# Performance work log

Measured on AMD Instinct MI355X. Metric: run time of the kernel, lower is better.

The kernel has to match this reference:

```python
import jax, jax.numpy as jnp
import numpy as np

K = 3
PAD = 1
K2 = K * K


def _deform_conv(x, offset, w, b):
    """torchvision-style DeformConv2d, stride=1, padding=1, kernel=3, dilation=1.
    x: [B,C,H,W]; offset: [B,2*K2,H,W] (per-tap (dy,dx) interleaved); w: [O,C,K,K]; b: [O].
    """
    B, C, H, W = x.shape
    # kernel tap offsets relative to center (padding=1 => taps at -1,0,1)
    ky = (jnp.arange(K) - PAD).astype(x.dtype)
    kx = (jnp.arange(K) - PAD).astype(x.dtype)
    ky = jnp.repeat(ky, K)   # [K2]
    kx = jnp.tile(kx, K)     # [K2]

    off = offset.reshape(B, K2, 2, H, W)
    # sampling coordinates: [B,K2,H,W]
    yy = off[:, :, 0] + ky[None, :, None, None] + jnp.arange(H, dtype=x.dtype)[None, None, :, None]
    xx = off[:, :, 1] + kx[None, :, None, None] + jnp.arange(W, dtype=x.dtype)[None, None, None, :]

    def sample_one(img, yb, xb):  # img [C,H,W]; yb,xb [K2,H,W]
        y0 = jnp.floor(yb)
        x0 = jnp.floor(xb)
        dy = yb - y0
        dx = xb - x0
        y0i = y0.astype(jnp.int32)
        x0i = x0.astype(jnp.int32)
        img_flat = img.reshape(C, -1)

        def gather(yi, xi):
            valid = (yi >= 0) & (yi < H) & (xi >= 0) & (xi < W)
            idx = jnp.clip(yi, 0, H - 1) * W + jnp.clip(xi, 0, W - 1)
            v = jnp.take(img_flat, idx.reshape(-1), axis=1).reshape(C, K2, H, W)
            return v * valid[None].astype(img.dtype)

        v00 = gather(y0i, x0i)
        v01 = gather(y0i, x0i + 1)
        v10 = gather(y0i + 1, x0i)
        v11 = gather(y0i + 1, x0i + 1)
        w00 = ((1 - dy) * (1 - dx))[None]
        w01 = ((1 - dy) * dx)[None]
        w10 = (dy * (1 - dx))[None]
        w11 = (dy * dx)[None]
        return v00 * w00 + v01 * w01 + v10 * w10 + v11 * w11  # [C,K2,H,W]

    samp = jax.vmap(sample_one)(x, yy, xx)  # [B,C,K2,H,W]
    wr = w.reshape(w.shape[0], C, K2)       # [O,C,K2]
    out = jnp.einsum('bckhw,ock->bohw', samp, wr)
    return out + b[None, :, None, None]


def setup_inputs() -> dict:
    key = jax.random.key(0)
    ks = jax.random.split(key, 8)
    B, Cin, H, W = 16, 256, 32, 32
    Ch, NC = 256, 1000
    fan1 = Cin * K2
    fan2 = Ch * K2
    return {
        'x': jax.random.normal(ks[0], (B, Cin, H, W), jnp.float32),
        'offset': jax.random.normal(ks[1], (B, 2 * K2, H, W), jnp.float32),
        'w1': jax.random.normal(ks[2], (Ch, Cin, K, K), jnp.float32) / np.sqrt(fan1),
        'b1': jnp.zeros((Ch,), jnp.float32),
        'w2': jax.random.normal(ks[3], (Ch, Ch, K, K), jnp.float32) / np.sqrt(fan2),
        'b2': jnp.zeros((Ch,), jnp.float32),
        'fc_w': jax.random.normal(ks[4], (NC, Ch), jnp.float32) / np.sqrt(Ch),
        'fc_b': jnp.zeros((NC,), jnp.float32),
    }


def reference(x, offset, w1, b1, w2, b2, fc_w, fc_b):
    h = jax.nn.relu(_deform_conv(x, offset, w1, b1))
    h = jax.nn.relu(_deform_conv(h, offset, w2, b2))
    pooled = h.mean(axis=(2, 3))            # adaptive_avg_pool2d to (1,1) then flatten
    return pooled @ fc_w.T + fc_b
```

## Files before the change

### kernel.cpp

```cpp
#include <hip/hip_runtime.h>

#define B_     16
#define C_     256
#define H_     32
#define W_     32
#define O_     256
#define K2_    9
#define HW_    1024
#define KTOT   2304
#define NPOS   16384
#define NCHUNK 288
#define NT     256

typedef __bf16 bf16;
typedef __attribute__((ext_vector_type(8))) __bf16 bf16x8;
typedef __attribute__((ext_vector_type(4))) float  f32x4;

__device__ __forceinline__ void gload_lds16(const bf16* g, bf16* l) {
    __builtin_amdgcn_global_load_lds(
        (const __attribute__((address_space(1))) void*)g,
        (__attribute__((address_space(3))) void*)l, 16, 0, 0);
}

__device__ __forceinline__ float4 load4(const float* p, int t) {
    return ((const float4*)p)[t];
}
__device__ __forceinline__ float4 load4(const bf16* p, int t) {
    const ushort4 u = ((const ushort4*)p)[t];
    float4 f;
    f.x = __uint_as_float((unsigned)u.x << 16);
    f.y = __uint_as_float((unsigned)u.y << 16);
    f.z = __uint_as_float((unsigned)u.z << 16);
    f.w = __uint_as_float((unsigned)u.w << 16);
    return f;
}

__global__ __launch_bounds__(256) void prep_w(
    const float* __restrict__ w, bf16* __restrict__ Wt)
{
    const int o    = blockIdx.x;
    const int om   = o >> 7, o128 = o & 127;
    for (int k = threadIdx.x; k < KTOT; k += 256) {
        const int cg  = k / 72;
        const int rem = k - cg * 72;
        const int tap = rem >> 3;
        const int cl  = rem & 7;
        const int c   = cg * 8 + cl;
        const int chunk = cg * 9 + tap;
        Wt[(((size_t)om * NCHUNK + chunk) * 128 + o128) * 8 + cl] =
            (bf16)w[((size_t)o * C_ + c) * K2_ + tap];
    }
}

template<typename T>
__global__ __launch_bounds__(256) void sample_kernel(
    const T* __restrict__ src, size_t c_stride, size_t b_stride,
    const float* __restrict__ off,
    bf16* __restrict__ S)
{
    __shared__ float4 xs4[2][1152];

    const int tid = threadIdx.x;
    const int cg  = blockIdx.x & 31;
    const int rq  = (blockIdx.x >> 5) & 3;
    const int b   = blockIdx.x >> 7;

    #pragma unroll
    for (int h = 0; h < 2; ++h) {
        const T* base = src + b * b_stride + (size_t)(cg * 8 + h * 4) * c_stride;
        const float4 v0 = load4(base,                tid);
        const float4 v1 = load4(base + c_stride,     tid);
        const float4 v2 = load4(base + 2 * c_stride, tid);
        const float4 v3 = load4(base + 3 * c_stride, tid);
        const int p0 = 4 * tid;
        xs4[h][(p0    ) + ((p0    ) >> 3)] = make_float4(v0.x, v1.x, v2.x, v3.x);
        xs4[h][(p0 + 1) + ((p0 + 1) >> 3)] = make_float4(v0.y, v1.y, v2.y, v3.y);
        xs4[h][(p0 + 2) + ((p0 + 2) >> 3)] = make_float4(v0.z, v1.z, v2.z, v3.z);
        xs4[h][(p0 + 3) + ((p0 + 3) >> 3)] = make_float4(v0.w, v1.w, v2.w, v3.w);
    }
    __syncthreads();

    for (int i = 0; i < 4; ++i) {
        const int rt   = rq * 4 + i;
        const int yrow = rt * 2;
        const int t    = b * 16 + rt;
        for (int item = tid; item < 576; item += 256) {
            const int pos = item & 63;
            const int tap = item >> 6;
            const int y   = yrow + (pos >> 5);
            const int x   = pos & 31;
            const float dyo = off[((b * 18 + 2 * tap)     << 10) + (y << 5) + x];
            const float dxo = off[((b * 18 + 2 * tap + 1) << 10) + (y << 5) + x];
            const float yy = dyo + (float)(tap / 3 - 1) + (float)y;
            const float xx = dxo + (float)(tap % 3 - 1) + (float)x;
            const float fy0 = floorf(yy), fx0 = floorf(xx);
            const float dy = yy - fy0, dx = xx - fx0;
            const int iy0 = (int)fy0, ix0 = (int)fx0;
            const int iy1 = iy0 + 1,  ix1 = ix0 + 1;
            const bool vy0 = (iy0 >= 0) && (iy0 < H_);
            const bool vy1 = (iy1 >= 0) && (iy1 < H_);
            const bool vx0 = (ix0 >= 0) && (ix0 < W_);
            const bool vx1 = (ix1 >= 0) && (ix1 < W_);
            const int cy0 = min(max(iy0, 0), H_ - 1), cy1 = min(max(iy1, 0), H_ - 1);
            const int cx0 = min(max(ix0, 0), W_ - 1), cx1 = min(max(ix1, 0), W_ - 1);
            const int p00 = cy0 * W_ + cx0, p01 = cy0 * W_ + cx1;
            const int p10 = cy1 * W_ + cx0, p11 = cy1 * W_ + cx1;
            const float w00 = (vy0 && vx0) ? (1.f - dy) * (1.f - dx) : 0.f;
            const float w01 = (vy0 && vx1) ? (1.f - dy) * dx         : 0.f;
            const float w10 = (vy1 && vx0) ? dy * (1.f - dx)         : 0.f;
            const float w11 = (vy1 && vx1) ? dy * dx                 : 0.f;
            const int s0 = p00 + (p00 >> 3);
            const int s1 = p01 + (p01 >> 3);
            const int s2 = p10 + (p10 >> 3);
            const int s3 = p11 + (p11 >> 3);
            bf16x8 v;
            #pragma unroll
            for (int h = 0; h < 2; ++h) {
                const float4 a = xs4[h][s0], bb = xs4[h][s1];
                const float4 c = xs4[h][s2], d  = xs4[h][s3];
                v[h * 4 + 0] = (bf16)(w00 * a.x + w01 * bb.x + w10 * c.x + w11 * d.x);
                v[h * 4 + 1] = (bf16)(w00 * a.y + w01 * bb.y + w10 * c.y + w11 * d.y);
                v[h * 4 + 2] = (bf16)(w00 * a.z + w01 * bb.z + w10 * c.z + w11 * d.z);
                v[h * 4 + 3] = (bf16)(w00 * a.w + w01 * bb.w + w10 * c.w + w11 * d.w);
            }
            const int chunk = cg * 9 + tap;
            *(bf16x8*)(S + (((size_t)t * NCHUNK + chunk) * 64 + pos) * 8) = v;
        }
    }
}

template<bool POOL>
__global__ __launch_bounds__(256) void gemm_kernel(
    const bf16* __restrict__ A,
    const bf16* __restrict__ Bm,
    const float* __restrict__ bias,
    bf16* __restrict__ F,
    float* __restrict__ pooled)
{
    __shared__ bf16 Al[8192];
    __shared__ bf16 Bl[4096];

    const int tid  = threadIdx.x;
    const int om   = blockIdx.x >> 8;
    const int pn   = blockIdx.x & 255;
    const int wave = tid >> 6, lane = tid & 63;
    const int wr   = wave >> 1, wc = wave & 1;
    const int l15  = lane & 15, l4 = lane >> 4;

    const bf16* Abase = A  + (size_t)om * NCHUNK * 128 * 8;
    const bf16* Bbase = Bm + (size_t)pn * NCHUNK * 64 * 8;

    f32x4 acc[4][2];
    #pragma unroll
    for (int m = 0; m < 4; ++m)
        #pragma unroll
        for (int n = 0; n < 2; ++n) acc[m][n] = (f32x4)0.f;

    for (int kt = 0; kt < NCHUNK / 8; ++kt) {
        __syncthreads();
        #pragma unroll
        for (int i = 0; i < 4; ++i)
            gload_lds16(Abase + (size_t)kt * 8192 + (i * 256 + tid) * 8,
                        &Al[(i * 256 + wave * 64) * 8]);
        #pragma unroll
        for (int i = 0; i < 2; ++i)
            gload_lds16(Bbase + (size_t)kt * 4096 + (i * 256 + tid) * 8,
                        &Bl[(i * 256 + wave * 64) * 8]);
        __syncthreads();

        #pragma unroll
        for (int ks = 0; ks < 2; ++ks) {
            const int cb = ks * 4 + l4;
            bf16x8 af[4], bq[2];
            #pragma unroll
            for (int m = 0; m < 4; ++m) {
                const int R = wr * 64 + m * 16 + l15;
                af[m] = *(const bf16x8*)&Al[(cb * 128 + R) * 8];
            }
            #pragma unroll
            for (int n = 0; n < 2; ++n) {
                const int R = wc * 32 + n * 16 + l15;
                bq[n] = *(const bf16x8*)&Bl[(cb * 64 + R) * 8];
            }
            #pragma unroll
            for (int m = 0; m < 4; ++m)
                #pragma unroll
                for (int n = 0; n < 2; ++n)
                    acc[m][n] = __builtin_amdgcn_mfma_f32_16x16x32_bf16(
                        af[m], bq[n], acc[m][n], 0, 0, 0);
        }
    }

    const int obase = om * 128 + wr * 64;
    if (!POOL) {
        #pragma unroll
        for (int m = 0; m < 4; ++m)
            #pragma unroll
            for (int j = 0; j < 4; ++j) {
                const int o  = obase + m * 16 + l4 * 4 + j;
                const float bb = bias[o];
                #pragma unroll
                for (int n = 0; n < 2; ++n) {
                    const int col = pn * 64 + wc * 32 + n * 16 + l15;
                    F[(size_t)o * NPOS + col] =
                        (bf16)fmaxf(acc[m][n][j] + bb, 0.f);
                }
            }
    } else {
        const int b = pn >> 4;
        #pragma unroll
        for (int m = 0; m < 4; ++m)
            #pragma unroll
            for (int j = 0; j < 4; ++j) {
                const int o  = obase + m * 16 + l4 * 4 + j;
                const float bb = bias[o];
                float s = fmaxf(acc[m][0][j] + bb, 0.f) +
                          fmaxf(acc[m][1][j] + bb, 0.f);
                s += __shfl_xor(s, 1);
                s += __shfl_xor(s, 2);
                s += __shfl_xor(s, 4);
                s += __shfl_xor(s, 8);
                if (l15 == 0)
                    atomicAdd(&pooled[b * 256 + o], s * (1.f / 1024.f));
            }
    }
}

__global__ __launch_bounds__(256) void fc_kernel(
    const float* __restrict__ pooled, const float* __restrict__ fw,
    const float* __restrict__ fb, float* __restrict__ out)
{
    __shared__ float pl[C_];
    const int b = blockIdx.x >> 2;
    const int q = blockIdx.x & 3;
    const int t = threadIdx.x;
    pl[t] = pooled[b * C_ + t];
    __syncthreads();
    const int n = q * 250 + t;
    if (t < 250) {
        const float4* wr = (const float4*)(fw + (size_t)n * C_);
        float s = 0.f;
        #pragma unroll 8
        for (int j = 0; j < C_ / 4; ++j) {
            const float4 v = wr[j];
            s += v.x * pl[4 * j] + v.y * pl[4 * j + 1] +
                 v.z * pl[4 * j + 2] + v.w * pl[4 * j + 3];
        }
        out[b * 1000 + n] = s + fb[n];
    }
}

extern "C" void kernel_launch(void* const* d_in, const int* in_sizes, int n_in,
                              void* d_out, int out_size, void* d_ws, size_t ws_size,
                              hipStream_t stream)
{
    const float* x   = (const float*)d_in[0];
    const float* off = (const float*)d_in[1];
    const float* w1  = (const float*)d_in[2];
    const float* b1  = (const float*)d_in[3];
    const float* w2  = (const float*)d_in[4];
    const float* b2  = (const float*)d_in[5];
    const float* fcw = (const float*)d_in[6];
    const float* fcb = (const float*)d_in[7];
    float* outp = (float*)d_out;

    bf16*  S      = (bf16*)d_ws;
    bf16*  F2     = S + (size_t)NPOS * KTOT;
    bf16*  Wt1    = F2 + (size_t)O_ * NPOS;
    bf16*  Wt2    = Wt1 + (size_t)O_ * KTOT;
    float* pooled = (float*)(Wt2 + (size_t)O_ * KTOT);

    prep_w<<<O_, 256, 0, stream>>>(w1, Wt1);
    prep_w<<<O_, 256, 0, stream>>>(w2, Wt2);
    hipMemsetAsync(pooled, 0, B_ * O_ * sizeof(float), stream);

    sample_kernel<float><<<2048, 256, 0, stream>>>(
        x, (size_t)HW_, (size_t)C_ * HW_, off, S);
    gemm_kernel<false><<<512, 256, 0, stream>>>(Wt1, S, b1, F2, nullptr);

    sample_kernel<bf16><<<2048, 256, 0, stream>>>(
        F2, (size_t)NPOS, (size_t)HW_, off, S);
    gemm_kernel<true><<<512, 256, 0, stream>>>(Wt2, S, b2, nullptr, pooled);

    fc_kernel<<<B_ * 4, 256, 0, stream>>>(pooled, fcw, fcb, outp);
}
```

Before: 207.5 us.

## Double-buffer GEMM LDS tiles, restructure sampling per thread, merge weight prep launches

The GEMM now uses two LDS buffers and issues the async global-to-LDS loads for the next k-tile before computing on the current one, so each iteration needs one barrier instead of two. The sampling kernel gives each thread a fixed output position, loads all 18 offsets into registers up front, and unrolls the 9 taps. It also gets an occupancy hint in its launch bounds. The two weight-prep launches and the memset are merged into one kernel. The trade-off is double the GEMM LDS footprint, which can lower occupancy, and more registers in the sampler.

```diff
diff --git a/kernel.cpp b/kernel.cpp
--- a/kernel.cpp
+++ b/kernel.cpp
@@ -10,7 +10,6 @@
 #define KTOT   2304
 #define NPOS   16384
 #define NCHUNK 288
-#define NT     256
 
 typedef __bf16 bf16;
 typedef __attribute__((ext_vector_type(8))) __bf16 bf16x8;
@@ -36,10 +35,16 @@
 }
 
 __global__ __launch_bounds__(256) void prep_w(
-    const float* __restrict__ w, bf16* __restrict__ Wt)
-{
-    const int o    = blockIdx.x;
-    const int om   = o >> 7, o128 = o & 127;
+    const float* __restrict__ w1, const float* __restrict__ w2,
+    bf16* __restrict__ Wt1, bf16* __restrict__ Wt2,
+    float* __restrict__ pooled)
+{
+    const int bx = blockIdx.x;
+    const float* w  = (bx < 256) ? w1 : w2;
+    bf16*      Wt   = (bx < 256) ? Wt1 : Wt2;
+    const int o     = bx & 255;
+    const int om    = o >> 7, o128 = o & 127;
+    if (bx < 16) pooled[bx * 256 + threadIdx.x] = 0.f;
     for (int k = threadIdx.x; k < KTOT; k += 256) {
         const int cg  = k / 72;
         const int rem = k - cg * 72;
@@ -53,7 +58,7 @@
 }
 
 template<typename T>
-__global__ __launch_bounds__(256) void sample_kernel(
+__global__ __launch_bounds__(256, 4) void sample_kernel(
     const T* __restrict__ src, size_t c_stride, size_t b_stride,
     const float* __restrict__ off,
     bf16* __restrict__ S)
@@ -78,54 +83,56 @@
         xs4[h][(p0 + 2) + ((p0 + 2) >> 3)] = make_float4(v0.z, v1.z, v2.z, v3.z);
         xs4[h][(p0 + 3) + ((p0 + 3) >> 3)] = make_float4(v0.w, v1.w, v2.w, v3.w);
     }
+
+    const int pos = tid & 63;
+    const int rt  = rq * 4 + (tid >> 6);
+    const int y   = rt * 2 + (pos >> 5);
+    const int x   = pos & 31;
+    const float* offb = off + ((size_t)(b * 18) << 10) + (y << 5) + x;
+    float dyo[9], dxo[9];
+    #pragma unroll
+    for (int k = 0; k < 9; ++k) {
+        dyo[k] = offb[(size_t)(2 * k) << 10];
+        dxo[k] = offb[((size_t)(2 * k) << 10) + 1024];
+    }
     __syncthreads();
 
-    for (int i = 0; i < 4; ++i) {
-        const int rt   = rq * 4 + i;
-        const int yrow = rt * 2;
-        const int t    = b * 16 + rt;
-        for (int item = tid; item < 576; item += 256) {
-            const int pos = item & 63;
-            const int tap = item >> 6;
-            const int y   = yrow + (pos >> 5);
-            const int x   = pos & 31;
-            const float dyo = off[((b * 18 + 2 * tap)     << 10) + (y << 5) + x];
-            const float dxo = off[((b * 18 + 2 * tap + 1) << 10) + (y << 5) + x];
-            const float yy = dyo + (float)(tap / 3 - 1) + (float)y;
-            const float xx = dxo + (float)(tap % 3 - 1) + (float)x;
-            const float fy0 = floorf(yy), fx0 = floorf(xx);
-            const float dy = yy - fy0, dx = xx - fx0;
-            const int iy0 = (int)fy0, ix0 = (int)fx0;
-            const int iy1 = iy0 + 1,  ix1 = ix0 + 1;
-            const bool vy0 = (iy0 >= 0) && (iy0 < H_);
-            const bool vy1 = (iy1 >= 0) && (iy1 < H_);
-            const bool vx0 = (ix0 >= 0) && (ix0 < W_);
-            const bool vx1 = (ix1 >= 0) && (ix1 < W_);
-            const int cy0 = min(max(iy0, 0), H_ - 1), cy1 = min(max(iy1, 0), H_ - 1);
-            const int cx0 = min(max(ix0, 0), W_ - 1), cx1 = min(max(ix1, 0), W_ - 1);
-            const int p00 = cy0 * W_ + cx0, p01 = cy0 * W_ + cx1;
-            const int p10 = cy1 * W_ + cx0, p11 = cy1 * W_ + cx1;
-            const float w00 = (vy0 && vx0) ? (1.f - dy) * (1.f - dx) : 0.f;
-            const float w01 = (vy0 && vx1) ? (1.f - dy) * dx         : 0.f;
-            const float w10 = (vy1 && vx0) ? dy * (1.f - dx)         : 0.f;
-            const float w11 = (vy1 && vx1) ? dy * dx                 : 0.f;
-            const int s0 = p00 + (p00 >> 3);
-            const int s1 = p01 + (p01 >> 3);
-            const int s2 = p10 + (p10 >> 3);
-            const int s3 = p11 + (p11 >> 3);
-            bf16x8 v;
-            #pragma unroll
-            for (int h = 0; h < 2; ++h) {
-                const float4 a = xs4[h][s0], bb = xs4[h][s1];
-                const float4 c = xs4[h][s2], d  = xs4[h][s3];
-                v[h * 4 + 0] = (bf16)(w00 * a.x + w01 * bb.x + w10 * c.x + w11 * d.x);
-                v[h * 4 + 1] = (bf16)(w00 * a.y + w01 * bb.y + w10 * c.y + w11 * d.y);
-                v[h * 4 + 2] = (bf16)(w00 * a.z + w01 * bb.z + w10 * c.z + w11 * d.z);
-                v[h * 4 + 3] = (bf16)(w00 * a.w + w01 * bb.w + w10 * c.w + w11 * d.w);
-            }
-            const int chunk = cg * 9 + tap;
-            *(bf16x8*)(S + (((size_t)t * NCHUNK + chunk) * 64 + pos) * 8) = v;
+    const size_t tbase = ((size_t)(b * 16 + rt) * NCHUNK + cg * 9) * 64 * 8;
+    #pragma unroll
+    for (int tap = 0; tap < 9; ++tap) {
+        const float yy = dyo[tap] + (float)(tap / 3 - 1) + (float)y;
+        const float xx = dxo[tap] + (float)(tap % 3 - 1) + (float)x;
+        const float fy0 = floorf(yy), fx0 = floorf(xx);
+        const float dy = yy - fy0, dx = xx - fx0;
+        const int iy0 = (int)fy0, ix0 = (int)fx0;
+        const int iy1 = iy0 + 1,  ix1 = ix0 + 1;
+        const bool vy0 = (iy0 >= 0) && (iy0 < H_);
+        const bool vy1 = (iy1 >= 0) && (iy1 < H_);
+        const bool vx0 = (ix0 >= 0) && (ix0 < W_);
+        const bool vx1 = (ix1 >= 0) && (ix1 < W_);
+        const int cy0 = min(max(iy0, 0), H_ - 1), cy1 = min(max(iy1, 0), H_ - 1);
+        const int cx0 = min(max(ix0, 0), W_ - 1), cx1 = min(max(ix1, 0), W_ - 1);
+        const int p00 = cy0 * W_ + cx0, p01 = cy0 * W_ + cx1;
+        const int p10 = cy1 * W_ + cx0, p11 = cy1 * W_ + cx1;
+        const float w00 = (vy0 && vx0) ? (1.f - dy) * (1.f - dx) : 0.f;
+        const float w01 = (vy0 && vx1) ? (1.f - dy) * dx         : 0.f;
+        const float w10 = (vy1 && vx0) ? dy * (1.f - dx)         : 0.f;
+        const float w11 = (vy1 && vx1) ? dy * dx                 : 0.f;
+        const int s0 = p00 + (p00 >> 3);
+        const int s1 = p01 + (p01 >> 3);
+        const int s2 = p10 + (p10 >> 3);
+        const int s3 = p11 + (p11 >> 3);
+        bf16x8 v;
+        #pragma unroll
+        for (int h = 0; h < 2; ++h) {
+            const float4 a = xs4[h][s0], bb = xs4[h][s1];
+            const float4 c = xs4[h][s2], d  = xs4[h][s3];
+            v[h * 4 + 0] = (bf16)(w00 * a.x + w01 * bb.x + w10 * c.x + w11 * d.x);
+            v[h * 4 + 1] = (bf16)(w00 * a.y + w01 * bb.y + w10 * c.y + w11 * d.y);
+            v[h * 4 + 2] = (bf16)(w00 * a.z + w01 * bb.z + w10 * c.z + w11 * d.z);
+            v[h * 4 + 3] = (bf16)(w00 * a.w + w01 * bb.w + w10 * c.w + w11 * d.w);
         }
+        *(bf16x8*)(S + tbase + (size_t)tap * 64 * 8 + pos * 8) = v;
     }
 }
 
@@ -137,8 +144,8 @@
     bf16* __restrict__ F,
     float* __restrict__ pooled)
 {
-    __shared__ bf16 Al[8192];
-    __shared__ bf16 Bl[4096];
+    __shared__ bf16 Al[2][8192];
+    __shared__ bf16 Bl[2][4096];
 
     const int tid  = threadIdx.x;
     const int om   = blockIdx.x >> 8;
@@ -156,17 +163,24 @@
         #pragma unroll
         for (int n = 0; n < 2; ++n) acc[m][n] = (f32x4)0.f;
 
+    #define STAGE(buf, kt)                                                    \
+        do {                                                                  \
+            _Pragma("unroll")                                                 \
+            for (int i = 0; i < 4; ++i)                                       \
+                gload_lds16(Abase + (size_t)(kt) * 8192 + (i * 256 + tid) * 8,\
+                            &Al[buf][(i * 256 + wave * 64) * 8]);             \
+            _Pragma("unroll")                                                 \
+            for (int i = 0; i < 2; ++i)                                       \
+                gload_lds16(Bbase + (size_t)(kt) * 4096 + (i * 256 + tid) * 8,\
+                            &Bl[buf][(i * 256 + wave * 64) * 8]);             \
+        } while (0)
+
+    STAGE(0, 0);
+    __syncthreads();
+
     for (int kt = 0; kt < NCHUNK / 8; ++kt) {
-        __syncthreads();
-        #pragma unroll
-        for (int i = 0; i < 4; ++i)
-            gload_lds16(Abase + (size_t)kt * 8192 + (i * 256 + tid) * 8,
-                        &Al[(i * 256 + wave * 64) * 8]);
-        #pragma unroll
-        for (int i = 0; i < 2; ++i)
-            gload_lds16(Bbase + (size_t)kt * 4096 + (i * 256 + tid) * 8,
-                        &Bl[(i * 256 + wave * 64) * 8]);
-        __syncthreads();
+        const int cur = kt & 1;
+        if (kt < NCHUNK / 8 - 1) STAGE(cur ^ 1, kt + 1);
 
         #pragma unroll
         for (int ks = 0; ks < 2; ++ks) {
@@ -175,12 +189,12 @@
             #pragma unroll
             for (int m = 0; m < 4; ++m) {
                 const int R = wr * 64 + m * 16 + l15;
-                af[m] = *(const bf16x8*)&Al[(cb * 128 + R) * 8];
+                af[m] = *(const bf16x8*)&Al[cur][(cb * 128 + R) * 8];
             }
             #pragma unroll
             for (int n = 0; n < 2; ++n) {
                 const int R = wc * 32 + n * 16 + l15;
-                bq[n] = *(const bf16x8*)&Bl[(cb * 64 + R) * 8];
+                bq[n] = *(const bf16x8*)&Bl[cur][(cb * 64 + R) * 8];
             }
             #pragma unroll
             for (int m = 0; m < 4; ++m)
@@ -189,7 +203,9 @@
                     acc[m][n] = __builtin_amdgcn_mfma_f32_16x16x32_bf16(
                         af[m], bq[n], acc[m][n], 0, 0, 0);
         }
-    }
+        __syncthreads();
+    }
+    #undef STAGE
 
     const int obase = om * 128 + wr * 64;
     if (!POOL) {
@@ -270,9 +286,7 @@
     bf16*  Wt2    = Wt1 + (size_t)O_ * KTOT;
     float* pooled = (float*)(Wt2 + (size_t)O_ * KTOT);
 
-    prep_w<<<O_, 256, 0, stream>>>(w1, Wt1);
-    prep_w<<<O_, 256, 0, stream>>>(w2, Wt2);
-    hipMemsetAsync(pooled, 0, B_ * O_ * sizeof(float), stream);
+    prep_w<<<512, 256, 0, stream>>>(w1, w2, Wt1, Wt2, pooled);
 
     sample_kernel<float><<<2048, 256, 0, stream>>>(
         x, (size_t)HW_, (size_t)C_ * HW_, off, S);
```

Result: no change. 207.8 us (+0.1%).
